# Kernel tuning notes

Measured on AMD Instinct MI355X. Metric: run time of the kernel, lower is better.

Reference implementation:

```python
import jax, jax.numpy as jnp
import numpy as np
import math

H = 768
NH = 12
DK = H // NH
EPS = 1e-12

def gelu(x):
    return 0.5 * x * (1 + jnp.tanh(math.sqrt(2 / math.pi) * (x + 0.044715 * x ** 3)))

def layernorm(x, w, b):
    u = x.mean(-1, keepdims=True)
    s = ((x - u) ** 2).mean(-1, keepdims=True)
    return w * (x - u) / jnp.sqrt(s + EPS) + b

def setup_inputs() -> dict:
    key = jax.random.key(0)
    ks = jax.random.split(key, 12)
    B, S = 4, 2048
    std = 1.0 / math.sqrt(H)
    inp = {
        'x': jax.random.normal(ks[0], (B, S, H), jnp.float32),
        'mask': jax.random.randint(ks[1], (B, S), 0, 2, jnp.int32),
        'wq': jax.random.normal(ks[2], (H, H), jnp.float32) * std,
        'wk': jax.random.normal(ks[3], (H, H), jnp.float32) * std,
        'wv': jax.random.normal(ks[4], (H, H), jnp.float32) * std,
        'wo': jax.random.normal(ks[5], (H, H), jnp.float32) * std,
        'wo_b': jnp.zeros((H,), jnp.float32),
        'w1': jax.random.normal(ks[6], (H, 4 * H), jnp.float32) * std,
        'w1_b': jnp.zeros((4 * H,), jnp.float32),
        'w2': jax.random.normal(ks[7], (4 * H, H), jnp.float32) * (0.5 / math.sqrt(H)),
        'w2_b': jnp.zeros((H,), jnp.float32),
        'ln1_w': jnp.ones((H,), jnp.float32),
        'ln1_b': jnp.zeros((H,), jnp.float32),
        'ln2_w': jnp.ones((H,), jnp.float32),
        'ln2_b': jnp.zeros((H,), jnp.float32),
    }
    return inp

def reference(x, mask, wq, wk, wv, wo, wo_b, w1, w1_b, w2, w2_b, ln1_w, ln1_b, ln2_w, ln2_b):
    B, S, _ = x.shape
    # --- attention sublayer (pre-LN, residual) ---
    y = layernorm(x, ln1_w, ln1_b)
    q = (y @ wq).reshape(B, S, NH, DK).transpose(0, 2, 1, 3)
    k = (y @ wk).reshape(B, S, NH, DK).transpose(0, 2, 1, 3)
    v = (y @ wv).reshape(B, S, NH, DK).transpose(0, 2, 1, 3)
    scores = jnp.einsum('bhqd,bhkd->bhqk', q, k) / math.sqrt(DK)
    m2 = (mask[:, :, None] * mask[:, None, :])[:, None, :, :]  # [B,1,S,S]
    scores = jnp.where(m2 == 0, jnp.float32(-1e9), scores)
    p = jax.nn.softmax(scores, axis=-1)
    ctx = jnp.einsum('bhqk,bhkd->bhqd', p, v).transpose(0, 2, 1, 3).reshape(B, S, H)
    x = x + ctx @ wo + wo_b
    # --- FFN sublayer ---
    y2 = layernorm(x, ln2_w, ln2_b)
    x = x + gelu(y2 @ w1 + w1_b) @ w2 + w2_b
    return x
```

## Files before the change

kernel.cpp:

```cpp
#include <hip/hip_runtime.h>
#include <hip/hip_bf16.h>

#define HD   768
#define BSZ  4
#define SEQ  2048
#define NTOK (BSZ*SEQ)
#define NHD  12
#define DKD  64

typedef __bf16 bf16_t;
typedef __bf16 bf16x8 __attribute__((ext_vector_type(8)));
typedef __bf16 bf16x4 __attribute__((ext_vector_type(4)));
typedef float  f32x4  __attribute__((ext_vector_type(4)));

__device__ __forceinline__ void async16(const void* g, void* l) {
    __builtin_amdgcn_global_load_lds(
        (const __attribute__((address_space(1))) unsigned int*)g,
        (__attribute__((address_space(3))) unsigned int*)l, 16, 0, 0);
}

__global__ __launch_bounds__(256) void wconv_kernel(
    const float* __restrict__ in, bf16_t* __restrict__ out, int K, int N)
{
    __shared__ float tile[32][33];
    const int k0 = blockIdx.y * 32, n0 = blockIdx.x * 32;
    const int t = threadIdx.x, r = t >> 5, c = t & 31;
#pragma unroll
    for (int j = 0; j < 4; j++)
        tile[r + 8*j][c] = in[(size_t)(k0 + r + 8*j) * N + n0 + c];
    __syncthreads();
#pragma unroll
    for (int j = 0; j < 4; j++)
        out[(size_t)(n0 + r + 8*j) * K + k0 + c] = (bf16_t)tile[c][r + 8*j];
}

__global__ __launch_bounds__(256) void mbias_kernel(
    const int* __restrict__ mask, float* __restrict__ mb)
{
    const int i = blockIdx.x * 256 + threadIdx.x;
    mb[i] = mask[i] ? 0.f : -1e9f;
}

__global__ __launch_bounds__(256) void ln_kernel(
    const float* __restrict__ x, const float* __restrict__ gw,
    const float* __restrict__ gb, bf16_t* __restrict__ y)
{
    const int row = blockIdx.x, t = threadIdx.x;
    const float* xr = x + (size_t)row * HD;
    float v0 = xr[t], v1 = xr[t + 256], v2 = xr[t + 512];
    float s1 = v0 + v1 + v2;
    float s2 = v0*v0 + v1*v1 + v2*v2;
#pragma unroll
    for (int m = 1; m < 64; m <<= 1) {
        s1 += __shfl_xor(s1, m);
        s2 += __shfl_xor(s2, m);
    }
    __shared__ float red[8];
    const int w = t >> 6, l = t & 63;
    if (l == 0) { red[w] = s1; red[4 + w] = s2; }
    __syncthreads();
    s1 = red[0] + red[1] + red[2] + red[3];
    s2 = red[4] + red[5] + red[6] + red[7];
    float mean = s1 * (1.f/HD);
    float var  = fmaxf(s2 * (1.f/HD) - mean*mean, 0.f);
    float rstd = rsqrtf(var + 1e-12f);
    bf16_t* yr = y + (size_t)row * HD;
    yr[t]       = (bf16_t)(gw[t]      * (v0 - mean) * rstd + gb[t]);
    yr[t + 256] = (bf16_t)(gw[t + 256]* (v1 - mean) * rstd + gb[t + 256]);
    yr[t + 512] = (bf16_t)(gw[t + 512]* (v2 - mean) * rstd + gb[t + 512]);
}

template<int EPI>
__global__ __launch_bounds__(256) void gemm_bt(
    const bf16_t* __restrict__ A, const bf16_t* __restrict__ BT,
    const float* __restrict__ bias, const float* __restrict__ resid,
    void* __restrict__ outv, int M, int N, int K, int ldo)
{
    __shared__ __align__(16) unsigned char lds[49152];
    const int t = threadIdx.x;
    const int w = t >> 6, l = t & 63;
    const int wr = w >> 1, wc = w & 1;
    const int lr = l & 15, lg = l >> 4;
    const int nwg = gridDim.x * gridDim.y;
    int flat = blockIdx.y * gridDim.x + blockIdx.x;
    flat = (flat & 7) * (nwg >> 3) + (flat >> 3);
    const int bx = flat % gridDim.x, by = flat / gridDim.x;
    const int m0 = by * 128, n0 = bx * 128;

    const bf16_t* a_src = A  + (size_t)(m0 + (t >> 2)) * K + (t & 3) * 8;
    const bf16_t* b_src = BT + (size_t)(n0 + (t >> 2)) * K + (t & 3) * 8;
    f32x4 acc[4][4] = {};

    auto stage = [&](int kt, int buf) {
        unsigned char* d = lds + buf * 16384 + t * 16;
        async16(a_src + kt,                 d);
        async16(a_src + (size_t)64*K + kt,  d + 4096);
        async16(b_src + kt,                 d + 8192);
        async16(b_src + (size_t)64*K + kt,  d + 12288);
    };

    const int nt = K >> 5;
    stage(0, 0);
    stage(32, 1);
    asm volatile("s_waitcnt vmcnt(4)" ::: "memory");
    __builtin_amdgcn_s_barrier();

    int cur = 0;
    for (int it = 0; it < nt; ++it) {
        const bool pre = (it + 2 < nt);
        if (pre) {
            int b2 = cur + 2; if (b2 >= 3) b2 -= 3;
            stage((it + 2) << 5, b2);
        }
        const unsigned char* bufp = lds + cur * 16384;
        bf16x8 af[4], bfr[4];
#pragma unroll
        for (int n = 0; n < 4; n++)
            bfr[n] = *(const bf16x8*)(bufp + 8192 + (wc*64 + n*16 + lr)*64 + lg*16);
#pragma unroll
        for (int m = 0; m < 4; m++)
            af[m] = *(const bf16x8*)(bufp + (wr*64 + m*16 + lr)*64 + lg*16);
        __builtin_amdgcn_s_setprio(1);
#pragma unroll
        for (int m = 0; m < 4; m++)
#pragma unroll
            for (int n = 0; n < 4; n++)
                acc[m][n] = __builtin_amdgcn_mfma_f32_16x16x32_bf16(af[m], bfr[n], acc[m][n], 0, 0, 0);
        __builtin_amdgcn_s_setprio(0);
        if (it + 1 < nt) {
            asm volatile("s_waitcnt lgkmcnt(0)" ::: "memory");
            if (pre) asm volatile("s_waitcnt vmcnt(4)" ::: "memory");
            else     asm volatile("s_waitcnt vmcnt(0)" ::: "memory");
            __builtin_amdgcn_s_barrier();
        }
        cur = (cur + 1 == 3) ? 0 : cur + 1;
    }

#pragma unroll
    for (int m = 0; m < 4; m++) {
#pragma unroll
        for (int n = 0; n < 4; n++) {
#pragma unroll
            for (int i = 0; i < 4; i++) {
                const int gr = m0 + wr*64 + m*16 + lg*4 + i;
                const int gc = n0 + wc*64 + n*16 + lr;
                float v = acc[m][n][i];
                if constexpr (EPI == 0) {
                    ((bf16_t*)outv)[(size_t)gr * ldo + gc] = (bf16_t)v;
                } else if constexpr (EPI == 1) {
                    ((float*)outv)[(size_t)gr * ldo + gc] =
                        v + bias[gc] + resid[(size_t)gr * ldo + gc];
                } else {
                    v += bias[gc];
                    float u = 0.7978845608028654f * (v + 0.044715f * v * v * v);
                    float g = v / (1.f + __expf(-2.f * u));
                    ((bf16_t*)outv)[(size_t)gr * ldo + gc] = (bf16_t)g;
                }
            }
        }
    }
}

__global__ __launch_bounds__(256) void vtrans_kernel(
    const bf16_t* __restrict__ qkv, bf16_t* __restrict__ vt)
{
    const int bh = blockIdx.y, b = bh / NHD, h = bh % NHD;
    const int s0 = blockIdx.x * 64;
    __shared__ bf16_t tile[64][72];
    const int t = threadIdx.x;
    {
        const int r = t >> 2, c0 = (t & 3) * 16;
        const bf16_t* src = qkv + (size_t)(b*SEQ + s0 + r) * 2304 + 1536 + h*64 + c0;
#pragma unroll
        for (int j = 0; j < 16; j++) tile[r][c0 + j] = src[j];
    }
    __syncthreads();
    {
        const int d = t >> 2, j0 = (t & 3) * 16;
        bf16_t* dst = vt + ((size_t)bh*64 + d) * SEQ + s0 + j0;
#pragma unroll
        for (int j = 0; j < 16; j++) dst[j] = tile[j0 + j][d];
    }
}

__global__ __launch_bounds__(256) void attn_kernel(
    const bf16_t* __restrict__ qkv, const bf16_t* __restrict__ vt,
    const int* __restrict__ mask, const float* __restrict__ mbias,
    bf16_t* __restrict__ ctx)
{
    __shared__ __align__(16) unsigned char lds[49152];
    const int t = threadIdx.x, w = t >> 6, l = t & 63;
    const int lr = l & 15, lg = l >> 4;
    int flat = blockIdx.y * 16 + blockIdx.x;
    flat = (flat & 7) * 96 + (flat >> 3);
    const int bh = flat >> 4, qt = flat & 15;
    const int b = bh / NHD, h = bh % NHD;
    const int q0 = qt * 128 + w * 32;
    const int swz = (lr & 7) << 4;

    bf16x8 qf[2][2];
#pragma unroll
    for (int r = 0; r < 2; r++)
#pragma unroll
        for (int ks = 0; ks < 2; ks++)
            qf[r][ks] = *(const bf16x8*)(qkv + (size_t)(b*SEQ + q0 + r*16 + lr)*2304
                                         + h*64 + ks*32 + lg*8);
    int mq[2];
#pragma unroll
    for (int r = 0; r < 2; r++)
        mq[r] = mask[b*SEQ + q0 + r*16 + lr];

    float mrow[2] = { -INFINITY, -INFINITY };
    float lsum[2] = { 0.f, 0.f };
    f32x4 accO[2][4] = {};

    auto stage_kv = [&](int kt, int buf) {
        unsigned char* d = lds + buf * 16384;
#pragma unroll
        for (int i2 = 0; i2 < 2; i2++) {
            const int c = i2*256 + t;
            const int row = c >> 3;
            const int scol = ((c & 7) ^ (row & 7)) * 8;
            async16(qkv + (size_t)(b*SEQ + kt + row)*2304 + 768 + h*64 + scol,
                    d + c*16);
            async16(vt + ((size_t)bh*64 + row)*SEQ + kt + scol,
                    d + 8192 + c*16);
        }
    };

    stage_kv(0, 0);
    __syncthreads();

    int cur = 0;
    for (int kt = 0; kt < SEQ; kt += 64) {
        if (kt + 64 < SEQ) stage_kv(kt + 64, cur ^ 1);
        f32x4 mb[4];
#pragma unroll
        for (int n = 0; n < 4; n++)
            mb[n] = *(const f32x4*)(mbias + (size_t)b*SEQ + kt + n*16 + lg*4);
        const unsigned char* bufp = lds + cur * 16384;

        bf16x8 kf[4][2];
#pragma unroll
        for (int n = 0; n < 4; n++)
#pragma unroll
            for (int ks = 0; ks < 2; ks++)
                kf[n][ks] = *(const bf16x8*)(bufp + (n*16 + lr)*128
                                             + ((ks*64 + lg*16) ^ swz));
        f32x4 accS[4][2] = {};
        __builtin_amdgcn_s_setprio(1);
#pragma unroll
        for (int n = 0; n < 4; n++)
#pragma unroll
            for (int r = 0; r < 2; r++)
#pragma unroll
                for (int ks = 0; ks < 2; ks++)
                    accS[n][r] = __builtin_amdgcn_mfma_f32_16x16x32_bf16(
                        kf[n][ks], qf[r][ks], accS[n][r], 0, 0, 0);
        __builtin_amdgcn_s_setprio(0);

#pragma unroll
        for (int r = 0; r < 2; r++) {
            f32x4 sl[4];
#pragma unroll
            for (int n = 0; n < 4; n++)
#pragma unroll
                for (int i = 0; i < 4; i++)
                    sl[n][i] = mq[r] ? (accS[n][r][i] * 0.125f + mb[n][i]) : -1e9f;
            float px = -INFINITY;
#pragma unroll
            for (int n = 0; n < 4; n++)
                px = fmaxf(px, fmaxf(fmaxf(sl[n][0], sl[n][1]),
                                     fmaxf(sl[n][2], sl[n][3])));
            px = fmaxf(px, __shfl_xor(px, 16));
            px = fmaxf(px, __shfl_xor(px, 32));
            const float mold = mrow[r];
            if (!__all(px <= mold + 8.f)) {
                const float mnew = fmaxf(mold, px);
                const float sc = __expf(mold - mnew);
                lsum[r] *= sc;
#pragma unroll
                for (int dn = 0; dn < 4; dn++) accO[r][dn] *= sc;
                mrow[r] = mnew;
            }
            const float m = mrow[r];
            float ps = 0.f;
#pragma unroll
            for (int n = 0; n < 4; n++) {
                bf16x4 pk;
#pragma unroll
                for (int i = 0; i < 4; i++) {
                    float pv = __expf(sl[n][i] - m);
                    ps += pv;
                    pk[i] = (bf16_t)pv;
                }
                *(bf16x4*)(lds + 32768 + w*4096 + (r*16 + lr)*128
                           + ((n*32 + lg*8) ^ swz)) = pk;
            }
            ps += __shfl_xor(ps, 16);
            ps += __shfl_xor(ps, 32);
            lsum[r] += ps;
        }

        bf16x8 vf[4][2], pf[2][2];
#pragma unroll
        for (int dn = 0; dn < 4; dn++)
#pragma unroll
            for (int ks = 0; ks < 2; ks++)
                vf[dn][ks] = *(const bf16x8*)(bufp + 8192 + (dn*16 + lr)*128
                                              + ((ks*64 + lg*16) ^ swz));
#pragma unroll
        for (int r = 0; r < 2; r++)
#pragma unroll
            for (int ks = 0; ks < 2; ks++)
                pf[r][ks] = *(const bf16x8*)(lds + 32768 + w*4096 + (r*16 + lr)*128
                                             + ((ks*64 + lg*16) ^ swz));
        __builtin_amdgcn_s_setprio(1);
#pragma unroll
        for (int r = 0; r < 2; r++)
#pragma unroll
            for (int dn = 0; dn < 4; dn++)
#pragma unroll
                for (int ks = 0; ks < 2; ks++)
                    accO[r][dn] = __builtin_amdgcn_mfma_f32_16x16x32_bf16(
                        vf[dn][ks], pf[r][ks], accO[r][dn], 0, 0, 0);
        __builtin_amdgcn_s_setprio(0);

        __syncthreads();
        cur ^= 1;
    }

#pragma unroll
    for (int r = 0; r < 2; r++) {
        const float inv = 1.f / lsum[r];
#pragma unroll
        for (int dn = 0; dn < 4; dn++) {
            bf16x4 ov;
#pragma unroll
            for (int i = 0; i < 4; i++)
                ov[i] = (bf16_t)(accO[r][dn][i] * inv);
            *(bf16x4*)(ctx + (size_t)(b*SEQ + q0 + r*16 + lr)*HD
                       + h*64 + dn*16 + lg*4) = ov;
        }
    }
}

extern "C" void kernel_launch(void* const* d_in, const int* in_sizes, int n_in,
                              void* d_out, int out_size, void* d_ws, size_t ws_size,
                              hipStream_t stream)
{
    const float* x     = (const float*)d_in[0];
    const int*   mask  = (const int*)  d_in[1];
    const float* wq    = (const float*)d_in[2];
    const float* wk    = (const float*)d_in[3];
    const float* wv    = (const float*)d_in[4];
    const float* wo    = (const float*)d_in[5];
    const float* wo_b  = (const float*)d_in[6];
    const float* w1    = (const float*)d_in[7];
    const float* w1_b  = (const float*)d_in[8];
    const float* w2    = (const float*)d_in[9];
    const float* w2_b  = (const float*)d_in[10];
    const float* ln1_w = (const float*)d_in[11];
    const float* ln1_b = (const float*)d_in[12];
    const float* ln2_w = (const float*)d_in[13];
    const float* ln2_b = (const float*)d_in[14];

    unsigned char* ws = (unsigned char*)d_ws;
    size_t o = 0;
    auto alloc = [&](size_t bytes) {
        size_t r = o; o += (bytes + 255) & ~(size_t)255; return r;
    };
    bf16_t* wqkvT = (bf16_t*)(ws + alloc((size_t)2304*768*2));
    bf16_t* woT   = (bf16_t*)(ws + alloc((size_t)768*768*2));
    bf16_t* w1T   = (bf16_t*)(ws + alloc((size_t)3072*768*2));
    bf16_t* w2T   = (bf16_t*)(ws + alloc((size_t)768*3072*2));
    bf16_t* y     = (bf16_t*)(ws + alloc((size_t)NTOK*HD*2));
    float*  x1    = (float*) (ws + alloc((size_t)NTOK*HD*4));
    bf16_t* ctx   = (bf16_t*)(ws + alloc((size_t)NTOK*HD*2));
    float*  mbias = (float*) (ws + alloc((size_t)NTOK*4));
    bf16_t* qkv   = (bf16_t*)(ws + alloc((size_t)NTOK*2304*2));
    bf16_t* vt    = (bf16_t*)(ws + alloc((size_t)48*64*SEQ*2));
    bf16_t* hbuf  = qkv;
    (void)in_sizes; (void)n_in; (void)out_size; (void)ws_size;

    wconv_kernel<<<dim3(24,24),256,0,stream>>>(wq, wqkvT,                 768, 768);
    wconv_kernel<<<dim3(24,24),256,0,stream>>>(wk, wqkvT + 768*768,       768, 768);
    wconv_kernel<<<dim3(24,24),256,0,stream>>>(wv, wqkvT + 2*768*768,     768, 768);
    wconv_kernel<<<dim3(24,24),256,0,stream>>>(wo, woT,                   768, 768);
    wconv_kernel<<<dim3(96,24),256,0,stream>>>(w1, w1T,                   768, 3072);
    wconv_kernel<<<dim3(24,96),256,0,stream>>>(w2, w2T,                   3072, 768);
    mbias_kernel<<<32,256,0,stream>>>(mask, mbias);

    ln_kernel<<<NTOK,256,0,stream>>>(x, ln1_w, ln1_b, y);
    gemm_bt<0><<<dim3(18,64),256,0,stream>>>(y, wqkvT, nullptr, nullptr, qkv,
                                             NTOK, 2304, 768, 2304);
    vtrans_kernel<<<dim3(32,48),256,0,stream>>>(qkv, vt);
    attn_kernel<<<dim3(16,48),256,0,stream>>>(qkv, vt, mask, mbias, ctx);
    gemm_bt<1><<<dim3(6,64),256,0,stream>>>(ctx, woT, wo_b, x, x1,
                                            NTOK, 768, 768, 768);
    ln_kernel<<<NTOK,256,0,stream>>>(x1, ln2_w, ln2_b, y);
    gemm_bt<2><<<dim3(24,64),256,0,stream>>>(y, w1T, w1_b, nullptr, hbuf,
                                             NTOK, 3072, 768, 3072);
    gemm_bt<1><<<dim3(6,64),256,0,stream>>>(hbuf, w2T, w2_b, x1, d_out,
                                            NTOK, 768, 3072, 768);
}
```

Measured before the change: 435.0 us.

## Fuse weight prep, write V transposed from QKV GEMM, load K/V directly in attention

Merges the six weight-conversion launches and the mask-bias launch into one prep kernel. The QKV GEMM now writes V columns straight into the transposed layout, which removes the separate V-transpose kernel. The attention kernel drops its LDS double-buffered async K/V staging and its per-tile barriers, and instead reads K and V fragments directly from global memory into registers, using LDS only for P. That cuts LDS use and synchronisation, but risks less coalesced, higher-latency global reads that are no longer overlapped with compute.

```diff
diff --git a/kernel.cpp b/kernel.cpp
--- a/kernel.cpp
+++ b/kernel.cpp
@@ -19,12 +19,40 @@
         (__attribute__((address_space(3))) unsigned int*)l, 16, 0, 0);
 }
 
-__global__ __launch_bounds__(256) void wconv_kernel(
-    const float* __restrict__ in, bf16_t* __restrict__ out, int K, int N)
-{
+__global__ __launch_bounds__(256) void prep_kernel(
+    const float* __restrict__ wq, const float* __restrict__ wk,
+    const float* __restrict__ wv, const float* __restrict__ wo,
+    const float* __restrict__ w1, const float* __restrict__ w2,
+    const int* __restrict__ mask,
+    bf16_t* __restrict__ wqkvT, bf16_t* __restrict__ woT,
+    bf16_t* __restrict__ w1T, bf16_t* __restrict__ w2T,
+    float* __restrict__ mb)
+{
+    const int bid = blockIdx.x, t = threadIdx.x;
+    if (bid >= 6912) {
+        const int i = (bid - 6912) * 256 + t;
+        mb[i] = mask[i] ? 0.f : -1e9f;
+        return;
+    }
+    const float* in; bf16_t* out; int K, N, ktile, ntile;
+    if (bid < 2304) {
+        const int wsel = bid / 576, tt = bid % 576;
+        const float* srcs[4] = { wq, wk, wv, wo };
+        bf16_t* dsts[4] = { wqkvT, wqkvT + 768*768, wqkvT + 2*768*768, woT };
+        in = srcs[wsel]; out = dsts[wsel]; K = 768; N = 768;
+        ktile = tt / 24; ntile = tt % 24;
+    } else if (bid < 4608) {
+        const int tt = bid - 2304;
+        in = w1; out = w1T; K = 768; N = 3072;
+        ktile = tt / 96; ntile = tt % 96;
+    } else {
+        const int tt = bid - 4608;
+        in = w2; out = w2T; K = 3072; N = 768;
+        ktile = tt / 24; ntile = tt % 24;
+    }
     __shared__ float tile[32][33];
-    const int k0 = blockIdx.y * 32, n0 = blockIdx.x * 32;
-    const int t = threadIdx.x, r = t >> 5, c = t & 31;
+    const int k0 = ktile * 32, n0 = ntile * 32;
+    const int r = t >> 5, c = t & 31;
 #pragma unroll
     for (int j = 0; j < 4; j++)
         tile[r + 8*j][c] = in[(size_t)(k0 + r + 8*j) * N + n0 + c];
@@ -32,13 +60,6 @@
 #pragma unroll
     for (int j = 0; j < 4; j++)
         out[(size_t)(n0 + r + 8*j) * K + k0 + c] = (bf16_t)tile[c][r + 8*j];
-}
-
-__global__ __launch_bounds__(256) void mbias_kernel(
-    const int* __restrict__ mask, float* __restrict__ mb)
-{
-    const int i = blockIdx.x * 256 + threadIdx.x;
-    mb[i] = mask[i] ? 0.f : -1e9f;
 }
 
 __global__ __launch_bounds__(256) void ln_kernel(
@@ -74,7 +95,8 @@
 __global__ __launch_bounds__(256) void gemm_bt(
     const bf16_t* __restrict__ A, const bf16_t* __restrict__ BT,
     const float* __restrict__ bias, const float* __restrict__ resid,
-    void* __restrict__ outv, int M, int N, int K, int ldo)
+    void* __restrict__ outv, int M, int N, int K, int ldo,
+    bf16_t* __restrict__ vtout)
 {
     __shared__ __align__(16) unsigned char lds[49152];
     const int t = threadIdx.x;
@@ -140,12 +162,24 @@
     for (int m = 0; m < 4; m++) {
 #pragma unroll
         for (int n = 0; n < 4; n++) {
+            const int gc  = n0 + wc*64 + n*16 + lr;
+            const int gr0 = m0 + wr*64 + m*16 + lg*4;
+            if constexpr (EPI == 3) {
+                if (gc >= 1536) {
+                    const int hh = (gc - 1536) >> 6, dd = (gc - 1536) & 63;
+                    const int bb = gr0 >> 11, ss = gr0 & 2047;
+                    bf16x4 ov;
+#pragma unroll
+                    for (int i = 0; i < 4; i++) ov[i] = (bf16_t)acc[m][n][i];
+                    *(bf16x4*)(vtout + ((size_t)(bb*NHD + hh)*64 + dd)*SEQ + ss) = ov;
+                    continue;
+                }
+            }
 #pragma unroll
             for (int i = 0; i < 4; i++) {
-                const int gr = m0 + wr*64 + m*16 + lg*4 + i;
-                const int gc = n0 + wc*64 + n*16 + lr;
+                const int gr = gr0 + i;
                 float v = acc[m][n][i];
-                if constexpr (EPI == 0) {
+                if constexpr (EPI == 0 || EPI == 3) {
                     ((bf16_t*)outv)[(size_t)gr * ldo + gc] = (bf16_t)v;
                 } else if constexpr (EPI == 1) {
                     ((float*)outv)[(size_t)gr * ldo + gc] =
@@ -161,34 +195,12 @@
     }
 }
 
-__global__ __launch_bounds__(256) void vtrans_kernel(
-    const bf16_t* __restrict__ qkv, bf16_t* __restrict__ vt)
-{
-    const int bh = blockIdx.y, b = bh / NHD, h = bh % NHD;
-    const int s0 = blockIdx.x * 64;
-    __shared__ bf16_t tile[64][72];
-    const int t = threadIdx.x;
-    {
-        const int r = t >> 2, c0 = (t & 3) * 16;
-        const bf16_t* src = qkv + (size_t)(b*SEQ + s0 + r) * 2304 + 1536 + h*64 + c0;
-#pragma unroll
-        for (int j = 0; j < 16; j++) tile[r][c0 + j] = src[j];
-    }
-    __syncthreads();
-    {
-        const int d = t >> 2, j0 = (t & 3) * 16;
-        bf16_t* dst = vt + ((size_t)bh*64 + d) * SEQ + s0 + j0;
-#pragma unroll
-        for (int j = 0; j < 16; j++) dst[j] = tile[j0 + j][d];
-    }
-}
-
 __global__ __launch_bounds__(256) void attn_kernel(
     const bf16_t* __restrict__ qkv, const bf16_t* __restrict__ vt,
     const int* __restrict__ mask, const float* __restrict__ mbias,
     bf16_t* __restrict__ ctx)
 {
-    __shared__ __align__(16) unsigned char lds[49152];
+    __shared__ __align__(16) unsigned char lds[16384];
     const int t = threadIdx.x, w = t >> 6, l = t & 63;
     const int lr = l & 15, lg = l >> 4;
     int flat = blockIdx.y * 16 + blockIdx.x;
@@ -214,39 +226,23 @@
     float lsum[2] = { 0.f, 0.f };
     f32x4 accO[2][4] = {};
 
-    auto stage_kv = [&](int kt, int buf) {
-        unsigned char* d = lds + buf * 16384;
-#pragma unroll
-        for (int i2 = 0; i2 < 2; i2++) {
-            const int c = i2*256 + t;
-            const int row = c >> 3;
-            const int scol = ((c & 7) ^ (row & 7)) * 8;
-            async16(qkv + (size_t)(b*SEQ + kt + row)*2304 + 768 + h*64 + scol,
-                    d + c*16);
-            async16(vt + ((size_t)bh*64 + row)*SEQ + kt + scol,
-                    d + 8192 + c*16);
-        }
-    };
-
-    stage_kv(0, 0);
-    __syncthreads();
-
-    int cur = 0;
+    const bf16_t* kbase = qkv + (size_t)(b*SEQ)*2304 + 768 + h*64 + lg*8;
+    const bf16_t* vbase = vt + (size_t)bh*64*SEQ + lg*8;
+    unsigned char* plds = lds + w*4096;
+
     for (int kt = 0; kt < SEQ; kt += 64) {
-        if (kt + 64 < SEQ) stage_kv(kt + 64, cur ^ 1);
+        bf16x8 kf[4][2];
+#pragma unroll
+        for (int n = 0; n < 4; n++)
+#pragma unroll
+            for (int ks = 0; ks < 2; ks++)
+                kf[n][ks] = *(const bf16x8*)(kbase
+                              + (size_t)(kt + n*16 + lr)*2304 + ks*32);
         f32x4 mb[4];
 #pragma unroll
         for (int n = 0; n < 4; n++)
             mb[n] = *(const f32x4*)(mbias + (size_t)b*SEQ + kt + n*16 + lg*4);
-        const unsigned char* bufp = lds + cur * 16384;
-
-        bf16x8 kf[4][2];
-#pragma unroll
-        for (int n = 0; n < 4; n++)
-#pragma unroll
-            for (int ks = 0; ks < 2; ks++)
-                kf[n][ks] = *(const bf16x8*)(bufp + (n*16 + lr)*128
-                                             + ((ks*64 + lg*16) ^ swz));
+
         f32x4 accS[4][2] = {};
         __builtin_amdgcn_s_setprio(1);
 #pragma unroll
@@ -258,6 +254,14 @@
                     accS[n][r] = __builtin_amdgcn_mfma_f32_16x16x32_bf16(
                         kf[n][ks], qf[r][ks], accS[n][r], 0, 0, 0);
         __builtin_amdgcn_s_setprio(0);
+
+        bf16x8 vf[4][2];
+#pragma unroll
+        for (int dn = 0; dn < 4; dn++)
+#pragma unroll
+            for (int ks = 0; ks < 2; ks++)
+                vf[dn][ks] = *(const bf16x8*)(vbase
+                               + (size_t)(dn*16 + lr)*SEQ + kt + ks*32);
 
 #pragma unroll
         for (int r = 0; r < 2; r++) {
@@ -294,26 +298,19 @@
                     ps += pv;
                     pk[i] = (bf16_t)pv;
                 }
-                *(bf16x4*)(lds + 32768 + w*4096 + (r*16 + lr)*128
-                           + ((n*32 + lg*8) ^ swz)) = pk;
+                *(bf16x4*)(plds + (r*16 + lr)*128 + ((n*32 + lg*8) ^ swz)) = pk;
             }
             ps += __shfl_xor(ps, 16);
             ps += __shfl_xor(ps, 32);
             lsum[r] += ps;
         }
 
-        bf16x8 vf[4][2], pf[2][2];
-#pragma unroll
-        for (int dn = 0; dn < 4; dn++)
+        bf16x8 pf[2][2];
+#pragma unroll
+        for (int r = 0; r < 2; r++)
 #pragma unroll
             for (int ks = 0; ks < 2; ks++)
-                vf[dn][ks] = *(const bf16x8*)(bufp + 8192 + (dn*16 + lr)*128
-                                              + ((ks*64 + lg*16) ^ swz));
-#pragma unroll
-        for (int r = 0; r < 2; r++)
-#pragma unroll
-            for (int ks = 0; ks < 2; ks++)
-                pf[r][ks] = *(const bf16x8*)(lds + 32768 + w*4096 + (r*16 + lr)*128
+                pf[r][ks] = *(const bf16x8*)(plds + (r*16 + lr)*128
                                              + ((ks*64 + lg*16) ^ swz));
         __builtin_amdgcn_s_setprio(1);
 #pragma unroll
@@ -325,9 +322,6 @@
                     accO[r][dn] = __builtin_amdgcn_mfma_f32_16x16x32_bf16(
                         vf[dn][ks], pf[r][ks], accO[r][dn], 0, 0, 0);
         __builtin_amdgcn_s_setprio(0);
-
-        __syncthreads();
-        cur ^= 1;
     }
 
 #pragma unroll
@@ -383,24 +377,17 @@
     bf16_t* hbuf  = qkv;
     (void)in_sizes; (void)n_in; (void)out_size; (void)ws_size;
 
-    wconv_kernel<<<dim3(24,24),256,0,stream>>>(wq, wqkvT,                 768, 768);
-    wconv_kernel<<<dim3(24,24),256,0,stream>>>(wk, wqkvT + 768*768,       768, 768);
-    wconv_kernel<<<dim3(24,24),256,0,stream>>>(wv, wqkvT + 2*768*768,     768, 768);
-    wconv_kernel<<<dim3(24,24),256,0,stream>>>(wo, woT,                   768, 768);
-    wconv_kernel<<<dim3(96,24),256,0,stream>>>(w1, w1T,                   768, 3072);
-    wconv_kernel<<<dim3(24,96),256,0,stream>>>(w2, w2T,                   3072, 768);
-    mbias_kernel<<<32,256,0,stream>>>(mask, mbias);
-
+    prep_kernel<<<6944,256,0,stream>>>(wq, wk, wv, wo, w1, w2, mask,
+                                       wqkvT, woT, w1T, w2T, mbias);
     ln_kernel<<<NTOK,256,0,stream>>>(x, ln1_w, ln1_b, y);
-    gemm_bt<0><<<dim3(18,64),256,0,stream>>>(y, wqkvT, nullptr, nullptr, qkv,
-                                             NTOK, 2304, 768, 2304);
-    vtrans_kernel<<<dim3(32,48),256,0,stream>>>(qkv, vt);
+    gemm_bt<3><<<dim3(18,64),256,0,stream>>>(y, wqkvT, nullptr, nullptr, qkv,
+                                             NTOK, 2304, 768, 2304, vt);
     attn_kernel<<<dim3(16,48),256,0,stream>>>(qkv, vt, mask, mbias, ctx);
     gemm_bt<1><<<dim3(6,64),256,0,stream>>>(ctx, woT, wo_b, x, x1,
-                                            NTOK, 768, 768, 768);
+                                            NTOK, 768, 768, 768, nullptr);
     ln_kernel<<<NTOK,256,0,stream>>>(x1, ln2_w, ln2_b, y);
     gemm_bt<2><<<dim3(24,64),256,0,stream>>>(y, w1T, w1_b, nullptr, hbuf,
-                                             NTOK, 3072, 768, 3072);
+                                             NTOK, 3072, 768, 3072, nullptr);
     gemm_bt<1><<<dim3(6,64),256,0,stream>>>(hbuf, w2T, w2_b, x1, d_out,
-                                            NTOK, 768, 3072, 768);
-}
+                                            NTOK, 768, 3072, 768, nullptr);
+}
```

Result: slower. 487.1 us (+12.0%).
